# Kernel tuning notes

Hardware: AMD Instinct MI355X
Metric: run time of the kernel (lower is better)

## Reference

```python
import jax, jax.numpy as jnp
import numpy as np


def _fwht_last(x):
    """Unnormalized Walsh-Hadamard transform along the last axis (len = power of 2)."""
    n = x.shape[-1]
    h = 1
    while h < n:
        x = x.reshape(*x.shape[:-1], n // (2 * h), 2, h)
        a, b = x[..., 0, :], x[..., 1, :]
        x = jnp.stack([a + b, a - b], axis=-2).reshape(*x.shape[:-3], n)
        h *= 2
    return x


def fwht(x, axis=-1):
    if axis in (-1, x.ndim - 1):
        return _fwht_last(x)
    return jnp.swapaxes(_fwht_last(jnp.swapaxes(x, axis, -1)), axis, -1)


def soft_threshold(x, T):
    return jnp.copysign(jax.nn.relu(jnp.abs(x) - jax.nn.relu(T)), x)


def setup_inputs() -> dict:
    key = jax.random.key(0)
    k1, k2, k3, k4 = jax.random.split(key, 4)
    B, C, H, W_dim = 32, 64, 128, 128
    x = jax.random.normal(k1, (B, C, H, W_dim), dtype=jnp.float32)
    W = jax.random.normal(k2, (C, C), dtype=jnp.float32) * 0.1  # 1x1 conv weight [out,in]
    v = jax.random.uniform(k3, (H, W_dim), dtype=jnp.float32)
    T = jax.random.uniform(k4, (H, W_dim), dtype=jnp.float32) * 0.1
    return {"x": x, "W": W, "v": v, "T": T}


def reference(x, W, v, T):
    H, Wd = x.shape[-2], x.shape[-1]
    # forward 2-D WHT (no padding: H, W already powers of 2)
    f2 = fwht(fwht(x, axis=-1), axis=-2)
    # spectral gate + 1x1 conv (channel mixing)
    f4 = jnp.einsum('oc,bchw->bohw', W, v * f2)
    # soft thresholding
    f6 = soft_threshold(f4, T)
    # inverse 2-D WHT = forward WHT / n along each axis
    y = fwht(fwht(f6, axis=-1), axis=-2) / (H * Wd)
    return y + x  # residual
```

## Files before the change

kernel.cpp:

```cpp
#include <hip/hip_runtime.h>
#include <math.h>

#define HW 16384
#define NPLANE 2048

typedef __bf16 bf16x8 __attribute__((ext_vector_type(8)));
typedef float  f32x4  __attribute__((ext_vector_type(4)));


__device__ __forceinline__ void bf_quad(float4& a) {
    float s0 = a.x + a.y, d0 = a.x - a.y;
    float s1 = a.z + a.w, d1 = a.z - a.w;
    a.x = s0 + s1; a.y = d0 + d1; a.z = s0 - s1; a.w = d0 - d1;
}

__device__ __forceinline__ void bf_pair(float4& a, float4& b) {
    float4 s, d;
    s.x = a.x + b.x; s.y = a.y + b.y; s.z = a.z + b.z; s.w = a.w + b.w;
    d.x = a.x - b.x; d.y = a.y - b.y; d.z = a.z - b.z; d.w = a.w - b.w;
    a = s; b = d;
}

__device__ __forceinline__ void bf_regs4(float4* r) {
    #pragma unroll
    for (int m = 1; m <= 8; m <<= 1) {
        #pragma unroll
        for (int j = 0; j < 16; ++j) {
            if ((j & m) == 0) bf_pair(r[j], r[j | m]);
        }
    }
}

__device__ __forceinline__ void wht16384(const float* __restrict__ src,
                                         float* __restrict__ lds,
                                         float4 (&r)[16],
                                         int l, int w) {
    const int l7 = l & 7, l3 = l >> 3;

    const int loadBase = w * 4096 + l * 4;
    #pragma unroll
    for (int j = 0; j < 16; ++j)
        r[j] = *reinterpret_cast<const float4*>(src + loadBase + j * 256);

    #pragma unroll
    for (int j = 0; j < 16; ++j) bf_quad(r[j]);
    bf_regs4(r);

    const int sA = w * 4096 + ((l7 ^ l3) << 2) + (l3 << 5);
    #pragma unroll
    for (int j = 0; j < 16; ++j)
        *reinterpret_cast<float4*>(lds + sA + j * 256) = r[j];
    __syncthreads();

    const int bB = (l7 << 5) + (l3 << 8) + ((w & 1) << 11) + ((w >> 1) << 13);
    #pragma unroll
    for (int j = 0; j < 16; ++j)
        r[j] = *reinterpret_cast<const float4*>(
            lds + bB + (((j & 7) ^ l7) << 2) + ((j >> 3) << 12));
    bf_regs4(r);
    #pragma unroll
    for (int j = 0; j < 16; ++j)
        *reinterpret_cast<float4*>(
            lds + bB + (((j & 7) ^ l7) << 2) + ((j >> 3) << 12)) = r[j];
    __syncthreads();

    const int bC = (l3 << 8) + (w << 11);
    #pragma unroll
    for (int j = 0; j < 16; ++j)
        r[j] = *reinterpret_cast<const float4*>(
            lds + bC + ((l7 ^ (j & 7)) << 2) + ((j & 7) << 5) + ((j >> 3) << 13));
    bf_regs4(r);
}

__global__ __launch_bounds__(256) void k_wht2d_fwd(const float* __restrict__ x,
                                                   float* __restrict__ out) {
    __shared__ float lds[HW];
    const int t = threadIdx.x;
    const int l = t & 63, w = t >> 6;
    const int l7 = l & 7, l3 = l >> 3;
    const size_t plane = (size_t)blockIdx.x * HW;

    float4 r[16];
    wht16384(x + plane, lds, r, l, w);

    float* dst = out + plane;
    const int oB = (l7 << 2) + (l3 << 8) + (w << 11);
    #pragma unroll
    for (int j = 0; j < 16; ++j)
        *reinterpret_cast<float4*>(dst + oB + ((j & 7) << 5) + ((j >> 3) << 13)) = r[j];
}

__global__ __launch_bounds__(256) void k_wht2d_inv(float* __restrict__ buf,
                                                   const float* __restrict__ x) {
    __shared__ float lds[HW];
    const int t = threadIdx.x;
    const int l = t & 63, w = t >> 6;
    const int l7 = l & 7, l3 = l >> 3;
    const size_t plane = (size_t)blockIdx.x * HW;

    float4 r[16];
    wht16384(buf + plane, lds, r, l, w);

    float* dst = buf + plane;
    const float* xr = x + plane;
    const float s = 1.0f / 16384.0f;
    const int oB = (l7 << 2) + (l3 << 8) + (w << 11);
    #pragma unroll
    for (int j = 0; j < 16; ++j) {
        const int off = oB + ((j & 7) << 5) + ((j >> 3) << 13);
        float4 xv = *reinterpret_cast<const float4*>(xr + off);
        float4 o;
        o.x = r[j].x * s + xv.x;
        o.y = r[j].y * s + xv.y;
        o.z = r[j].z * s + xv.z;
        o.w = r[j].w * s + xv.w;
        *reinterpret_cast<float4*>(dst + off) = o;
    }
}

__global__ __launch_bounds__(256) void k_mix_mfma(float* __restrict__ buf,
                                                  const float* __restrict__ W,
                                                  const float* __restrict__ v,
                                                  const float* __restrict__ T) {
    __shared__ float Xs[64 * 128];
    const int t = threadIdx.x;
    const int l = t & 63, w = t >> 6;
    const int b  = blockIdx.x >> 7;
    const int p0 = (blockIdx.x & 127) << 7;
    float* base = buf + (size_t)b * 64 * HW + p0;

    bf16x8 A[4][2];
    {
        const int row = l & 15;
        const int kc  = (l >> 4) * 8;
        #pragma unroll
        for (int mt = 0; mt < 4; ++mt) {
            const float* wr = W + (mt * 16 + row) * 64 + kc;
            #pragma unroll
            for (int ks = 0; ks < 2; ++ks) {
                float4 w0 = *reinterpret_cast<const float4*>(wr + ks * 32);
                float4 w1 = *reinterpret_cast<const float4*>(wr + ks * 32 + 4);
                bf16x8 a;
                a[0] = (__bf16)w0.x; a[1] = (__bf16)w0.y;
                a[2] = (__bf16)w0.z; a[3] = (__bf16)w0.w;
                a[4] = (__bf16)w1.x; a[5] = (__bf16)w1.y;
                a[6] = (__bf16)w1.z; a[7] = (__bf16)w1.w;
                A[mt][ks] = a;
            }
        }
    }

    #pragma unroll
    for (int i = 0; i < 8; ++i) {
        const int d  = i * 1024 + t * 4;
        const int c  = d >> 7;
        const int pq = d & 127;
        float4 xv = *reinterpret_cast<const float4*>(base + (size_t)c * HW + pq);
        float4 vv = *reinterpret_cast<const float4*>(v + p0 + pq);
        float4 r;
        r.x = xv.x * vv.x; r.y = xv.y * vv.y;
        r.z = xv.z * vv.z; r.w = xv.w * vv.w;
        const int gc = (c >> 3) & 3;
        *reinterpret_cast<float4*>(Xs + c * 128 + (pq ^ (gc << 4))) = r;
    }
    __syncthreads();

    f32x4 acc[4][2] = {};
    const int n0 = w * 32;
    const int g  = l >> 4;
    #pragma unroll
    for (int nt = 0; nt < 2; ++nt) {
        const int pl = n0 + nt * 16 + (l & 15);
        #pragma unroll
        for (int ks = 0; ks < 2; ++ks) {
            const float* col = Xs + (ks * 32 + g * 8) * 128 + (pl ^ (g << 4));
            bf16x8 bb;
            #pragma unroll
            for (int j = 0; j < 8; ++j) bb[j] = (__bf16)col[j * 128];
            #pragma unroll
            for (int mt = 0; mt < 4; ++mt)
                acc[mt][nt] = __builtin_amdgcn_mfma_f32_16x16x32_bf16(
                    A[mt][ks], bb, acc[mt][nt], 0, 0, 0);
        }
    }

    #pragma unroll
    for (int nt = 0; nt < 2; ++nt) {
        const int p  = p0 + n0 + nt * 16 + (l & 15);
        const float Tp = fmaxf(T[p], 0.0f);
        #pragma unroll
        for (int mt = 0; mt < 4; ++mt) {
            #pragma unroll
            for (int r = 0; r < 4; ++r) {
                const int o = mt * 16 + g * 4 + r;
                float val = acc[mt][nt][r];
                float mag = fmaxf(fabsf(val) - Tp, 0.0f);
                buf[(size_t)b * 64 * HW + (size_t)o * HW + p] = copysignf(mag, val);
            }
        }
    }
}

extern "C" void kernel_launch(void* const* d_in, const int* in_sizes, int n_in,
                              void* d_out, int out_size, void* d_ws, size_t ws_size,
                              hipStream_t stream) {
    const float* x = (const float*)d_in[0];
    const float* W = (const float*)d_in[1];
    const float* v = (const float*)d_in[2];
    const float* T = (const float*)d_in[3];
    float* out = (float*)d_out;

    k_wht2d_fwd<<<NPLANE, 256, 0, stream>>>(x, out);
    k_mix_mfma<<<32 * 128, 256, 0, stream>>>(out, W, v, T);
    k_wht2d_inv<<<NPLANE, 256, 0, stream>>>(out, x);
}
```

Before: 150.4 us.

## Restructure 2-D WHT kernels to 512 threads with 8 float4 registers each

Rewrites the per-plane 16384-point Walsh-Hadamard transform so each of 512 threads holds 8 float4 values instead of 256 threads holding 16. The butterfly stages are regrouped into three register passes with new swizzled LDS layouts and scalar-strided LDS accesses, and outputs are written as float2 stores. The aim is to halve register pressure and double threads per plane for more latency hiding. In exchange it adds more LDS traffic granularity, narrower global stores and harder-to-verify index mappings.

```diff
diff --git a/kernel.cpp b/kernel.cpp
--- a/kernel.cpp
+++ b/kernel.cpp
@@ -21,100 +21,140 @@
     a = s; b = d;
 }
 
-__device__ __forceinline__ void bf_regs4(float4* r) {
-    #pragma unroll
-    for (int m = 1; m <= 8; m <<= 1) {
-        #pragma unroll
-        for (int j = 0; j < 16; ++j) {
-            if ((j & m) == 0) bf_pair(r[j], r[j | m]);
-        }
-    }
-}
-
-__device__ __forceinline__ void wht16384(const float* __restrict__ src,
-                                         float* __restrict__ lds,
-                                         float4 (&r)[16],
-                                         int l, int w) {
-    const int l7 = l & 7, l3 = l >> 3;
-
-    const int loadBase = w * 4096 + l * 4;
-    #pragma unroll
-    for (int j = 0; j < 16; ++j)
-        r[j] = *reinterpret_cast<const float4*>(src + loadBase + j * 256);
-
-    #pragma unroll
-    for (int j = 0; j < 16; ++j) bf_quad(r[j]);
-    bf_regs4(r);
-
-    const int sA = w * 4096 + ((l7 ^ l3) << 2) + (l3 << 5);
-    #pragma unroll
-    for (int j = 0; j < 16; ++j)
-        *reinterpret_cast<float4*>(lds + sA + j * 256) = r[j];
+__device__ __forceinline__ void bf_regs3(float4 (&r)[8]) {
+    #pragma unroll
+    for (int m = 1; m <= 4; m <<= 1) {
+        #pragma unroll
+        for (int j = 0; j < 8; ++j) {
+            if (!(j & m)) bf_pair(r[j], r[j | m]);
+        }
+    }
+}
+
+__device__ __forceinline__ void wht14(const float* __restrict__ src,
+                                      float* __restrict__ lds,
+                                      float4 (&r)[8], int t) {
+    const float4* s4 = reinterpret_cast<const float4*>(src);
+    #pragma unroll
+    for (int j = 0; j < 8; ++j) r[j] = s4[t + j * 512];
+    #pragma unroll
+    for (int j = 0; j < 8; ++j) bf_quad(r[j]);
+    bf_regs3(r);
+
+    {
+        const int physT = (t & 3)
+                        + ((((t >> 5) ^ (t >> 4)) & 1) << 4)
+                        + (((t >> 6) & 7) << 5)
+                        + (((t >> 2) & 7) << 8);
+        const int swc = (t >> 2) & 3;
+        #pragma unroll
+        for (int j = 0; j < 8; ++j) {
+            float* b = lds + physT + j * 2048;
+            b[(0 ^ swc) << 2] = r[j].x;
+            b[(1 ^ swc) << 2] = r[j].y;
+            b[(2 ^ swc) << 2] = r[j].z;
+            b[(3 ^ swc) << 2] = r[j].w;
+        }
+    }
     __syncthreads();
 
-    const int bB = (l7 << 5) + (l3 << 8) + ((w & 1) << 11) + ((w >> 1) << 13);
-    #pragma unroll
-    for (int j = 0; j < 16; ++j)
-        r[j] = *reinterpret_cast<const float4*>(
-            lds + bB + (((j & 7) ^ l7) << 2) + ((j >> 3) << 12));
-    bf_regs4(r);
-    #pragma unroll
-    for (int j = 0; j < 16; ++j)
-        *reinterpret_cast<float4*>(
-            lds + bB + (((j & 7) ^ l7) << 2) + ((j >> 3) << 12)) = r[j];
+    {
+        const int baseT = ((t & 63) << 2) + ((t >> 6) << 11);
+        int addr[8];
+        #pragma unroll
+        for (int j = 0; j < 8; ++j) {
+            addr[j] = (baseT ^ ((j & 3) << 2) ^ ((j >> 2) << 4)) + (j << 8);
+            r[j] = *reinterpret_cast<const float4*>(lds + addr[j]);
+        }
+        #pragma unroll
+        for (int j = 0; j < 8; ++j) bf_quad(r[j]);
+        bf_regs3(r);
+        #pragma unroll
+        for (int j = 0; j < 8; ++j)
+            *reinterpret_cast<float4*>(lds + addr[j]) = r[j];
+    }
     __syncthreads();
 
-    const int bC = (l3 << 8) + (w << 11);
-    #pragma unroll
-    for (int j = 0; j < 16; ++j)
-        r[j] = *reinterpret_cast<const float4*>(
-            lds + bC + ((l7 ^ (j & 7)) << 2) + ((j & 7) << 5) + ((j >> 3) << 13));
-    bf_regs4(r);
-}
-
-__global__ __launch_bounds__(256) void k_wht2d_fwd(const float* __restrict__ x,
+    {
+        const int t0 = t & 1, t1 = (t >> 1) & 1, t2 = (t >> 2) & 1;
+        const int t3 = (t >> 3) & 1, t4 = (t >> 4) & 1, t5 = (t >> 5) & 1;
+        const int cT = t1 + (t2 << 1) + ((t0 ^ t4) << 3)
+                     + (t3 << 8) + (t4 << 9) + (t5 << 10) + ((t >> 6) << 11);
+        #pragma unroll
+        for (int j = 0; j < 8; ++j) {
+            const int a = cT + ((((j >> 2) ^ t3)) << 2)
+                        + ((j & 1) << 6) + (((j >> 1) & 1) << 7);
+            float4 q;
+            q.x = lds[a + ((0 ^ t5) << 4)];
+            q.y = lds[a + ((1 ^ t5) << 4)];
+            q.z = lds[a + ((0 ^ t5) << 4) + (1 << 5)];
+            q.w = lds[a + ((1 ^ t5) << 4) + (1 << 5)];
+            r[j] = q;
+        }
+        #pragma unroll
+        for (int j = 0; j < 8; ++j) bf_quad(r[j]);
+        #pragma unroll
+        for (int m = 1; m <= 2; m <<= 1) {
+            #pragma unroll
+            for (int j = 0; j < 8; ++j) {
+                if (!(j & m)) bf_pair(r[j], r[j | m]);
+            }
+        }
+    }
+}
+
+__global__ __launch_bounds__(512) void k_wht2d_fwd(const float* __restrict__ x,
                                                    float* __restrict__ out) {
     __shared__ float lds[HW];
     const int t = threadIdx.x;
-    const int l = t & 63, w = t >> 6;
-    const int l7 = l & 7, l3 = l >> 3;
     const size_t plane = (size_t)blockIdx.x * HW;
 
-    float4 r[16];
-    wht16384(x + plane, lds, r, l, w);
+    float4 r[8];
+    wht14(x + plane, lds, r, t);
 
     float* dst = out + plane;
-    const int oB = (l7 << 2) + (l3 << 8) + (w << 11);
-    #pragma unroll
-    for (int j = 0; j < 16; ++j)
-        *reinterpret_cast<float4*>(dst + oB + ((j & 7) << 5) + ((j >> 3) << 13)) = r[j];
-}
-
-__global__ __launch_bounds__(256) void k_wht2d_inv(float* __restrict__ buf,
+    const int dT = ((t & 63) << 1) + ((t >> 6) << 11);
+    #pragma unroll
+    for (int j = 0; j < 4; ++j) {
+        const int jb = dT + ((j & 1) << 9) + ((j >> 1) << 10);
+        const float* lo = reinterpret_cast<const float*>(&r[j]);
+        const float* hi = reinterpret_cast<const float*>(&r[j + 4]);
+        #pragma unroll
+        for (int c = 0; c < 4; ++c) {
+            const int d = jb + ((c & 1) << 7) + ((c >> 1) << 8);
+            float2 o; o.x = lo[c]; o.y = hi[c];
+            *reinterpret_cast<float2*>(dst + d) = o;
+        }
+    }
+}
+
+__global__ __launch_bounds__(512) void k_wht2d_inv(float* __restrict__ buf,
                                                    const float* __restrict__ x) {
     __shared__ float lds[HW];
     const int t = threadIdx.x;
-    const int l = t & 63, w = t >> 6;
-    const int l7 = l & 7, l3 = l >> 3;
     const size_t plane = (size_t)blockIdx.x * HW;
 
-    float4 r[16];
-    wht16384(buf + plane, lds, r, l, w);
+    float4 r[8];
+    wht14(buf + plane, lds, r, t);
 
     float* dst = buf + plane;
     const float* xr = x + plane;
     const float s = 1.0f / 16384.0f;
-    const int oB = (l7 << 2) + (l3 << 8) + (w << 11);
-    #pragma unroll
-    for (int j = 0; j < 16; ++j) {
-        const int off = oB + ((j & 7) << 5) + ((j >> 3) << 13);
-        float4 xv = *reinterpret_cast<const float4*>(xr + off);
-        float4 o;
-        o.x = r[j].x * s + xv.x;
-        o.y = r[j].y * s + xv.y;
-        o.z = r[j].z * s + xv.z;
-        o.w = r[j].w * s + xv.w;
-        *reinterpret_cast<float4*>(dst + off) = o;
+    const int dT = ((t & 63) << 1) + ((t >> 6) << 11);
+    #pragma unroll
+    for (int j = 0; j < 4; ++j) {
+        const int jb = dT + ((j & 1) << 9) + ((j >> 1) << 10);
+        const float* lo = reinterpret_cast<const float*>(&r[j]);
+        const float* hi = reinterpret_cast<const float*>(&r[j + 4]);
+        #pragma unroll
+        for (int c = 0; c < 4; ++c) {
+            const int d = jb + ((c & 1) << 7) + ((c >> 1) << 8);
+            float2 xv = *reinterpret_cast<const float2*>(xr + d);
+            float2 o;
+            o.x = lo[c] * s + xv.x;
+            o.y = hi[c] * s + xv.y;
+            *reinterpret_cast<float2*>(dst + d) = o;
+        }
     }
 }
 
@@ -210,7 +250,7 @@
     const float* T = (const float*)d_in[3];
     float* out = (float*)d_out;
 
-    k_wht2d_fwd<<<NPLANE, 256, 0, stream>>>(x, out);
+    k_wht2d_fwd<<<NPLANE, 512, 0, stream>>>(x, out);
     k_mix_mfma<<<32 * 128, 256, 0, stream>>>(out, W, v, T);
-    k_wht2d_inv<<<NPLANE, 256, 0, stream>>>(out, x);
-}
+    k_wht2d_inv<<<NPLANE, 512, 0, stream>>>(out, x);
+}
```

After: 151.1 us. No clear change (+0.5%).

## Store intermediate spectra as bf16 and stage WHT in fp16 LDS

Applied to the files above, without the earlier changes.

Forward WHT now writes the spectrum as bf16 into the first half of each output plane slot, with the spectral gate v folded in. The mix kernel reads and writes bf16, and the inverse kernel reads bf16 and applies the 1/n scale before the transform. LDS staging uses packed fp16 (half the LDS, allowing 4 blocks per CU) with a new three-stage butterfly and swizzle layout. This cuts global traffic for the intermediate buffers and raises occupancy, at the cost of precision in both the spectrum and the in-LDS butterflies (fp16 range and rounding).

```diff
diff --git a/kernel.cpp b/kernel.cpp
--- a/kernel.cpp
+++ b/kernel.cpp
@@ -3,17 +3,34 @@
 
 #define HW 16384
 #define NPLANE 2048
-
+#define SLOTB 65536ull
+
+typedef __fp16 f16x2 __attribute__((ext_vector_type(2)));
 typedef __bf16 bf16x8 __attribute__((ext_vector_type(8)));
 typedef float  f32x4  __attribute__((ext_vector_type(4)));
 
+__device__ __forceinline__ unsigned pk16(float a, float b) {
+    f16x2 h = __builtin_amdgcn_cvt_pkrtz(a, b);
+    return __builtin_bit_cast(unsigned, h);
+}
+__device__ __forceinline__ float2 up16(unsigned u) {
+    f16x2 h = __builtin_bit_cast(f16x2, u);
+    return make_float2((float)h[0], (float)h[1]);
+}
+__device__ __forceinline__ float bf2f(unsigned short s) {
+    unsigned u = (unsigned)s << 16;
+    return __builtin_bit_cast(float, u);
+}
+__device__ __forceinline__ unsigned short f2bf(float f) {
+    __bf16 h = (__bf16)f;
+    return __builtin_bit_cast(unsigned short, h);
+}
 
 __device__ __forceinline__ void bf_quad(float4& a) {
     float s0 = a.x + a.y, d0 = a.x - a.y;
     float s1 = a.z + a.w, d1 = a.z - a.w;
     a.x = s0 + s1; a.y = d0 + d1; a.z = s0 - s1; a.w = d0 - d1;
 }
-
 __device__ __forceinline__ void bf_pair(float4& a, float4& b) {
     float4 s, d;
     s.x = a.x + b.x; s.y = a.y + b.y; s.z = a.z + b.z; s.w = a.w + b.w;
@@ -21,113 +38,165 @@
     a = s; b = d;
 }
 
-__device__ __forceinline__ void bf_regs4(float4* r) {
+__device__ __forceinline__ void wht_ABC(float4 (&r)[16], unsigned* lds, int t,
+                                        float4 (&c)[16]) {
+    const int t0 = t & 1, t1 = (t >> 1) & 1, t2 = (t >> 2) & 1, t3 = (t >> 3) & 1;
+    const int t4 = (t >> 4) & 1, t5 = (t >> 5) & 1, t6 = (t >> 6) & 1;
+    const int thi = t >> 4;
+
+    #pragma unroll
+    for (int j = 0; j < 16; ++j) bf_quad(r[j]);
     #pragma unroll
     for (int m = 1; m <= 8; m <<= 1) {
         #pragma unroll
         for (int j = 0; j < 16; ++j) {
-            if ((j & m) == 0) bf_pair(r[j], r[j | m]);
-        }
-    }
-}
-
-__device__ __forceinline__ void wht16384(const float* __restrict__ src,
-                                         float* __restrict__ lds,
-                                         float4 (&r)[16],
-                                         int l, int w) {
-    const int l7 = l & 7, l3 = l >> 3;
-
-    const int loadBase = w * 4096 + l * 4;
-    #pragma unroll
-    for (int j = 0; j < 16; ++j)
-        r[j] = *reinterpret_cast<const float4*>(src + loadBase + j * 256);
-
-    #pragma unroll
-    for (int j = 0; j < 16; ++j) bf_quad(r[j]);
-    bf_regs4(r);
-
-    const int sA = w * 4096 + ((l7 ^ l3) << 2) + (l3 << 5);
-    #pragma unroll
-    for (int j = 0; j < 16; ++j)
-        *reinterpret_cast<float4*>(lds + sA + j * 256) = r[j];
+            if (!(j & m)) bf_pair(r[j], r[j | m]);
+        }
+    }
+    const int wA = (t0 << 1) | ((t1 ^ t4) << 2) | ((t2 ^ t5) << 3)
+                 | ((t3 ^ t6) << 4) | (thi << 5);
+    #pragma unroll
+    for (int j = 0; j < 16; ++j) {
+        uint2 u;
+        u.x = pk16(r[j].x, r[j].y);
+        u.y = pk16(r[j].z, r[j].w);
+        *reinterpret_cast<uint2*>(lds + wA + (j << 9)) = u;
+    }
     __syncthreads();
 
-    const int bB = (l7 << 5) + (l3 << 8) + ((w & 1) << 11) + ((w >> 1) << 13);
-    #pragma unroll
-    for (int j = 0; j < 16; ++j)
-        r[j] = *reinterpret_cast<const float4*>(
-            lds + bB + (((j & 7) ^ l7) << 2) + ((j >> 3) << 12));
-    bf_regs4(r);
-    #pragma unroll
-    for (int j = 0; j < 16; ++j)
-        *reinterpret_cast<float4*>(
-            lds + bB + (((j & 7) ^ l7) << 2) + ((j >> 3) << 12)) = r[j];
+    float e[8][8];
+    const int wB = ((t & 15) << 5) | (thi << 9);
+    int wb[8];
+    #pragma unroll
+    for (int j = 0; j < 8; ++j) {
+        wb[j] = wB | ((j ^ (t & 7)) << 2);
+        uint4 u = *reinterpret_cast<const uint4*>(lds + wb[j]);
+        float2 f0 = up16(u.x), f1 = up16(u.y), f2 = up16(u.z), f3 = up16(u.w);
+        e[j][0] = f0.x; e[j][1] = f0.y; e[j][2] = f1.x; e[j][3] = f1.y;
+        e[j][4] = f2.x; e[j][5] = f2.y; e[j][6] = f3.x; e[j][7] = f3.y;
+    }
+    #pragma unroll
+    for (int j = 0; j < 8; ++j) {
+        #pragma unroll
+        for (int q = 0; q < 4; ++q) {
+            float a = e[j][q], b = e[j][q + 4];
+            e[j][q] = a + b; e[j][q + 4] = a - b;
+        }
+    }
+    #pragma unroll
+    for (int m = 1; m <= 4; m <<= 1) {
+        #pragma unroll
+        for (int j = 0; j < 8; ++j) {
+            if (!(j & m)) {
+                #pragma unroll
+                for (int q = 0; q < 8; ++q) {
+                    float a = e[j][q], b = e[j | m][q];
+                    e[j][q] = a + b; e[j | m][q] = a - b;
+                }
+            }
+        }
+    }
+    #pragma unroll
+    for (int j = 0; j < 8; ++j) {
+        uint4 u;
+        u.x = pk16(e[j][0], e[j][1]);
+        u.y = pk16(e[j][2], e[j][3]);
+        u.z = pk16(e[j][4], e[j][5]);
+        u.w = pk16(e[j][6], e[j][7]);
+        *reinterpret_cast<uint4*>(lds + wb[j]) = u;
+    }
     __syncthreads();
 
-    const int bC = (l3 << 8) + (w << 11);
-    #pragma unroll
-    for (int j = 0; j < 16; ++j)
-        r[j] = *reinterpret_cast<const float4*>(
-            lds + bC + ((l7 ^ (j & 7)) << 2) + ((j & 7) << 5) + ((j >> 3) << 13));
-    bf_regs4(r);
-}
-
-__global__ __launch_bounds__(256) void k_wht2d_fwd(const float* __restrict__ x,
-                                                   float* __restrict__ out) {
-    __shared__ float lds[HW];
+    const int wC = (t0 << 1) | (thi << 9);
+    const int tm = (t >> 1) & 7;
+    #pragma unroll
+    for (int k = 0; k < 16; ++k) {
+        const int w = wC | (((k & 7) ^ tm) << 2) | (k << 5);
+        uint2 u = *reinterpret_cast<const uint2*>(lds + w);
+        float2 f0 = up16(u.x), f1 = up16(u.y);
+        c[k].x = f0.x; c[k].y = f0.y; c[k].z = f1.x; c[k].w = f1.y;
+    }
+    #pragma unroll
+    for (int m = 1; m <= 8; m <<= 1) {
+        #pragma unroll
+        for (int k = 0; k < 16; ++k) {
+            if (!(k & m)) bf_pair(c[k], c[k | m]);
+        }
+    }
+}
+
+__global__ __launch_bounds__(256, 4) void k_fwd(const float* __restrict__ x,
+                                                void* outbuf,
+                                                const float* __restrict__ v) {
+    __shared__ unsigned lds[8192];
     const int t = threadIdx.x;
-    const int l = t & 63, w = t >> 6;
-    const int l7 = l & 7, l3 = l >> 3;
-    const size_t plane = (size_t)blockIdx.x * HW;
+    const int plane = blockIdx.x;
+    const float4* s4 = reinterpret_cast<const float4*>(x + (size_t)plane * HW);
 
     float4 r[16];
-    wht16384(x + plane, lds, r, l, w);
-
-    float* dst = out + plane;
-    const int oB = (l7 << 2) + (l3 << 8) + (w << 11);
-    #pragma unroll
-    for (int j = 0; j < 16; ++j)
-        *reinterpret_cast<float4*>(dst + oB + ((j & 7) << 5) + ((j >> 3) << 13)) = r[j];
-}
-
-__global__ __launch_bounds__(256) void k_wht2d_inv(float* __restrict__ buf,
-                                                   const float* __restrict__ x) {
-    __shared__ float lds[HW];
+    #pragma unroll
+    for (int j = 0; j < 16; ++j) r[j] = s4[t + j * 256];
+
+    float4 c[16];
+    wht_ABC(r, lds, t, c);
+
+    ushort4* dst = reinterpret_cast<ushort4*>((char*)outbuf + (size_t)plane * SLOTB);
+    const int obase = (t & 15) + ((t >> 4) << 8);
+    #pragma unroll
+    for (int k = 0; k < 16; ++k) {
+        const int o4 = obase + (k << 4);
+        const float4 vv = *reinterpret_cast<const float4*>(v + (o4 << 2));
+        ushort4 u;
+        u.x = f2bf(c[k].x * vv.x);
+        u.y = f2bf(c[k].y * vv.y);
+        u.z = f2bf(c[k].z * vv.z);
+        u.w = f2bf(c[k].w * vv.w);
+        dst[o4] = u;
+    }
+}
+
+__global__ __launch_bounds__(256, 4) void k_inv(void* outbuf,
+                                                const float* __restrict__ x) {
+    __shared__ unsigned lds[8192];
     const int t = threadIdx.x;
-    const int l = t & 63, w = t >> 6;
-    const int l7 = l & 7, l3 = l >> 3;
-    const size_t plane = (size_t)blockIdx.x * HW;
+    const int plane = blockIdx.x;
+    const float sc = 1.0f / 16384.0f;
+    const ushort4* src =
+        reinterpret_cast<const ushort4*>((const char*)outbuf + (size_t)plane * SLOTB);
 
     float4 r[16];
-    wht16384(buf + plane, lds, r, l, w);
-
-    float* dst = buf + plane;
-    const float* xr = x + plane;
-    const float s = 1.0f / 16384.0f;
-    const int oB = (l7 << 2) + (l3 << 8) + (w << 11);
     #pragma unroll
     for (int j = 0; j < 16; ++j) {
-        const int off = oB + ((j & 7) << 5) + ((j >> 3) << 13);
-        float4 xv = *reinterpret_cast<const float4*>(xr + off);
+        ushort4 u = src[t + j * 256];
+        r[j].x = bf2f(u.x) * sc; r[j].y = bf2f(u.y) * sc;
+        r[j].z = bf2f(u.z) * sc; r[j].w = bf2f(u.w) * sc;
+    }
+
+    float4 c[16];
+    wht_ABC(r, lds, t, c);
+
+    float* dst = reinterpret_cast<float*>((char*)outbuf + (size_t)plane * SLOTB);
+    const float* xr = x + (size_t)plane * HW;
+    const int obase = (t & 15) + ((t >> 4) << 8);
+    #pragma unroll
+    for (int k = 0; k < 16; ++k) {
+        const int o4 = obase + (k << 4);
+        float4 xv = *reinterpret_cast<const float4*>(xr + (o4 << 2));
         float4 o;
-        o.x = r[j].x * s + xv.x;
-        o.y = r[j].y * s + xv.y;
-        o.z = r[j].z * s + xv.z;
-        o.w = r[j].w * s + xv.w;
-        *reinterpret_cast<float4*>(dst + off) = o;
-    }
-}
-
-__global__ __launch_bounds__(256) void k_mix_mfma(float* __restrict__ buf,
+        o.x = c[k].x + xv.x; o.y = c[k].y + xv.y;
+        o.z = c[k].z + xv.z; o.w = c[k].w + xv.w;
+        *reinterpret_cast<float4*>(dst + (o4 << 2)) = o;
+    }
+}
+
+__global__ __launch_bounds__(256) void k_mix_mfma(void* buf,
                                                   const float* __restrict__ W,
-                                                  const float* __restrict__ v,
                                                   const float* __restrict__ T) {
     __shared__ float Xs[64 * 128];
     const int t = threadIdx.x;
     const int l = t & 63, w = t >> 6;
     const int b  = blockIdx.x >> 7;
     const int p0 = (blockIdx.x & 127) << 7;
-    float* base = buf + (size_t)b * 64 * HW + p0;
 
     bf16x8 A[4][2];
     {
@@ -153,15 +222,15 @@
     #pragma unroll
     for (int i = 0; i < 8; ++i) {
         const int d  = i * 1024 + t * 4;
-        const int c  = d >> 7;
+        const int cc = d >> 7;
         const int pq = d & 127;
-        float4 xv = *reinterpret_cast<const float4*>(base + (size_t)c * HW + pq);
-        float4 vv = *reinterpret_cast<const float4*>(v + p0 + pq);
+        const ushort4* src = reinterpret_cast<const ushort4*>(
+            (const char*)buf + (size_t)(b * 64 + cc) * SLOTB);
+        ushort4 u = src[(p0 + pq) >> 2];
         float4 r;
-        r.x = xv.x * vv.x; r.y = xv.y * vv.y;
-        r.z = xv.z * vv.z; r.w = xv.w * vv.w;
-        const int gc = (c >> 3) & 3;
-        *reinterpret_cast<float4*>(Xs + c * 128 + (pq ^ (gc << 4))) = r;
+        r.x = bf2f(u.x); r.y = bf2f(u.y); r.z = bf2f(u.z); r.w = bf2f(u.w);
+        const int gc = (cc >> 3) & 3;
+        *reinterpret_cast<float4*>(Xs + cc * 128 + (pq ^ (gc << 4))) = r;
     }
     __syncthreads();
 
@@ -190,12 +259,14 @@
         const float Tp = fmaxf(T[p], 0.0f);
         #pragma unroll
         for (int mt = 0; mt < 4; ++mt) {
+            unsigned short* orow = reinterpret_cast<unsigned short*>(
+                (char*)buf + (size_t)(b * 64 + mt * 16 + g * 4) * SLOTB);
             #pragma unroll
             for (int r = 0; r < 4; ++r) {
-                const int o = mt * 16 + g * 4 + r;
                 float val = acc[mt][nt][r];
                 float mag = fmaxf(fabsf(val) - Tp, 0.0f);
-                buf[(size_t)b * 64 * HW + (size_t)o * HW + p] = copysignf(mag, val);
+                reinterpret_cast<unsigned short*>(
+                    (char*)orow + (size_t)r * SLOTB)[p] = f2bf(copysignf(mag, val));
             }
         }
     }
@@ -208,9 +279,8 @@
     const float* W = (const float*)d_in[1];
     const float* v = (const float*)d_in[2];
     const float* T = (const float*)d_in[3];
-    float* out = (float*)d_out;
-
-    k_wht2d_fwd<<<NPLANE, 256, 0, stream>>>(x, out);
-    k_mix_mfma<<<32 * 128, 256, 0, stream>>>(out, W, v, T);
-    k_wht2d_inv<<<NPLANE, 256, 0, stream>>>(out, x);
-}
+
+    k_fwd<<<NPLANE, 256, 0, stream>>>(x, d_out, v);
+    k_mix_mfma<<<32 * 128, 256, 0, stream>>>(d_out, W, T);
+    k_inv<<<NPLANE, 256, 0, stream>>>(d_out, x);
+}
```

After: 145.1 us. 1.04x faster.
